# Optimization experiments

Measured on AMD Instinct MI355X. Metric: run time of the kernel, lower is better.

Reference implementation:

```python
import jax, jax.numpy as jnp
import numpy as np
from math import sqrt

B, S, E, H = 4, 4096, 512, 64


def setup_inputs() -> dict:
    key = jax.random.key(0)
    ks = jax.random.split(key, 9)
    std = sqrt(2.0 / (E + 4 * H))
    x_query = jax.random.normal(ks[0], (B, S, E), dtype=jnp.float32)
    x_key = jax.random.normal(ks[1], (B, S, E), dtype=jnp.float32)
    x_value = jax.random.normal(ks[2], (B, S, E), dtype=jnp.float32)
    Wq = jax.random.normal(ks[3], (E, H), dtype=jnp.float32) * std
    Wk = jax.random.normal(ks[4], (E, H), dtype=jnp.float32) * std
    Wv = jax.random.normal(ks[5], (E, H), dtype=jnp.float32) * std
    bq = jnp.zeros((H,), dtype=jnp.float32)
    bk = jnp.zeros((H,), dtype=jnp.float32)
    bv = jnp.zeros((H,), dtype=jnp.float32)
    # causal mask: True entries are masked out (set to -inf), as in scores[mask] = -inf
    mask = jnp.broadcast_to(jnp.triu(jnp.ones((S, S), dtype=bool), k=1), (B, S, S))
    return {"x_query": x_query, "x_key": x_key, "x_value": x_value,
            "Wq": Wq, "bq": bq, "Wk": Wk, "bk": bk, "Wv": Wv, "bv": bv,
            "mask": mask}


def reference(x_query, x_key, x_value, Wq, bq, Wk, bk, Wv, bv, mask):
    scale = 1.0 / sqrt(H)
    Q = x_query @ Wq + bq              # [B, S, H]
    K = x_key @ Wk + bk                # [B, S, H]
    V = x_value @ Wv + bv              # [B, S, H]
    scores = jnp.einsum('bqh,bkh->bqk', Q, K) * scale  # [B, S, S]
    scores = jnp.where(mask, -jnp.inf, scores)
    attn = jax.nn.softmax(scores, axis=-1)
    Z = jnp.einsum('bqk,bkh->bqh', attn, V)             # [B, S, H]
    return Z
```

## Files before the change

kernel.cpp:

```cpp
#include <hip/hip_runtime.h>
#include <math.h>

#define BB 4
#define SS 4096
#define EE 512
#define HH 64
#define NSPLIT 8
#define NQ (BB * SS)

typedef __bf16 bf16x8 __attribute__((ext_vector_type(8)));
typedef short  s16x8  __attribute__((ext_vector_type(8)));
typedef float  f32x4  __attribute__((ext_vector_type(4)));

static __device__ __forceinline__ unsigned short f2bf(float f) {
    union { float f; unsigned int u; } v; v.f = f;
    unsigned int r = v.u + 0x7fffu + ((v.u >> 16) & 1u);
    return (unsigned short)(r >> 16);
}
static __device__ __forceinline__ float bf2f(unsigned short h) {
    union { unsigned int u; float f; } v; v.u = ((unsigned int)h) << 16;
    return v.f;
}
static __device__ __forceinline__ void split_bf(float x, unsigned short& h, unsigned short& l) {
    h = f2bf(x);
    l = f2bf(x - bf2f(h));
}

static __device__ __forceinline__ f32x4 mfma_bf16(s16x8 a, s16x8 b, f32x4 c) {
    return __builtin_amdgcn_mfma_f32_16x16x32_bf16(
        __builtin_bit_cast(bf16x8, a), __builtin_bit_cast(bf16x8, b), c, 0, 0, 0);
}

__global__ __launch_bounds__(256) void wprep_kernel(
    const float* __restrict__ Wq, const float* __restrict__ Wk,
    const float* __restrict__ Wv,
    unsigned short* __restrict__ WhT, unsigned short* __restrict__ WlT)
{
    const int mat = blockIdx.y;
    const float* W = (mat == 0) ? Wq : ((mat == 1) ? Wk : Wv);
    const int base = blockIdx.x * 2048;
    for (int ii = threadIdx.x; ii < 2048; ii += 256) {
        const int i = base + ii;
        const int k = i >> 6, n = i & 63;
        unsigned short h, l;
        split_bf(W[i], h, l);
        const size_t o = ((size_t)mat * HH + n) * EE + k;
        WhT[o] = h; WlT[o] = l;
    }
}

__global__ __launch_bounds__(256) void qkv_proj_kernel(
    const float* __restrict__ Xq, const float* __restrict__ Xk, const float* __restrict__ Xv,
    const float* __restrict__ bq, const float* __restrict__ bk, const float* __restrict__ bv,
    const unsigned short* __restrict__ WhT, const unsigned short* __restrict__ WlT,
    unsigned short* __restrict__ Qbf, unsigned short* __restrict__ Kbf,
    unsigned short* __restrict__ Vtb)
{
    const int mtx = blockIdx.y;
    const float* X    = (mtx == 0) ? Xq : ((mtx == 1) ? Xk : Xv);
    const float* bias = (mtx == 0) ? bq : ((mtx == 1) ? bk : bv);

    __shared__ unsigned short Ah[64 * 72], Al[64 * 72];
    __shared__ unsigned short Bh[64 * 72], Bl[64 * 72];

    const int tid  = threadIdx.x;
    const int lane = tid & 63;
    const int w    = tid >> 6;
    const int l15  = lane & 15;
    const int lg   = lane >> 4;
    const int r0   = blockIdx.x * 64;

    const int arow = tid >> 2;
    const int asg  = tid & 3;

    f32x4 acc[4] = {{0,0,0,0},{0,0,0,0},{0,0,0,0},{0,0,0,0}};

    for (int c = 0; c < EE / 64; ++c) {
        const float* xp = &X[(size_t)(r0 + arow) * EE + c * 64 + asg * 16];
        const float4 x0 = ((const float4*)xp)[0];
        const float4 x1 = ((const float4*)xp)[1];
        const float4 x2 = ((const float4*)xp)[2];
        const float4 x3 = ((const float4*)xp)[3];
        const size_t wb = ((size_t)mtx * HH + arow) * EE + (size_t)c * 64;
        const s16x8 wh0 = *(const s16x8*)&WhT[wb + asg * 8];
        const s16x8 wh1 = *(const s16x8*)&WhT[wb + 32 + asg * 8];
        const s16x8 wl0 = *(const s16x8*)&WlT[wb + asg * 8];
        const s16x8 wl1 = *(const s16x8*)&WlT[wb + 32 + asg * 8];
        __syncthreads();

        const float xs[16] = {x0.x,x0.y,x0.z,x0.w, x1.x,x1.y,x1.z,x1.w,
                              x2.x,x2.y,x2.z,x2.w, x3.x,x3.y,x3.z,x3.w};
        s16x8 ha, hb, la, lb;
        #pragma unroll
        for (int i = 0; i < 8; ++i) {
            unsigned short h, l;
            split_bf(xs[i], h, l);      ha[i] = (short)h; la[i] = (short)l;
            split_bf(xs[8 + i], h, l);  hb[i] = (short)h; lb[i] = (short)l;
        }
        *(s16x8*)&Ah[arow * 72 + asg * 16]     = ha;
        *(s16x8*)&Ah[arow * 72 + asg * 16 + 8] = hb;
        *(s16x8*)&Al[arow * 72 + asg * 16]     = la;
        *(s16x8*)&Al[arow * 72 + asg * 16 + 8] = lb;
        *(s16x8*)&Bh[arow * 72 + asg * 8]      = wh0;
        *(s16x8*)&Bh[arow * 72 + 32 + asg * 8] = wh1;
        *(s16x8*)&Bl[arow * 72 + asg * 8]      = wl0;
        *(s16x8*)&Bl[arow * 72 + 32 + asg * 8] = wl1;
        __syncthreads();

        const int ma = (w * 16 + l15) * 72;
        const s16x8 a_h0 = *(const s16x8*)&Ah[ma + lg * 8];
        const s16x8 a_h1 = *(const s16x8*)&Ah[ma + 32 + lg * 8];
        const s16x8 a_l0 = *(const s16x8*)&Al[ma + lg * 8];
        const s16x8 a_l1 = *(const s16x8*)&Al[ma + 32 + lg * 8];
        #pragma unroll
        for (int f = 0; f < 4; ++f) {
            const int nb = (f * 16 + l15) * 72;
            const s16x8 b_h0 = *(const s16x8*)&Bh[nb + lg * 8];
            const s16x8 b_h1 = *(const s16x8*)&Bh[nb + 32 + lg * 8];
            const s16x8 b_l0 = *(const s16x8*)&Bl[nb + lg * 8];
            const s16x8 b_l1 = *(const s16x8*)&Bl[nb + 32 + lg * 8];
            acc[f] = mfma_bf16(a_h0, b_h0, acc[f]);
            acc[f] = mfma_bf16(a_h1, b_h1, acc[f]);
            acc[f] = mfma_bf16(a_l0, b_h0, acc[f]);
            acc[f] = mfma_bf16(a_l1, b_h1, acc[f]);
            acc[f] = mfma_bf16(a_h0, b_l0, acc[f]);
            acc[f] = mfma_bf16(a_h1, b_l1, acc[f]);
        }
    }

    float bcol[4];
    #pragma unroll
    for (int f = 0; f < 4; ++f) bcol[f] = bias[f * 16 + l15];

    if (mtx < 2) {
        unsigned short* Out = (mtx == 0) ? Qbf : Kbf;
        #pragma unroll
        for (int f = 0; f < 4; ++f)
            #pragma unroll
            for (int r = 0; r < 4; ++r)
                Out[(size_t)(r0 + w * 16 + lg * 4 + r) * HH + f * 16 + l15] =
                    f2bf(acc[f][r] + bcol[f]);
    } else {
        const int b  = r0 >> 12;
        const int s0 = (r0 & 4095) + w * 16 + lg * 4;
        #pragma unroll
        for (int f = 0; f < 4; ++f) {
            ushort4 pk;
            pk.x = f2bf(acc[f][0] + bcol[f]);
            pk.y = f2bf(acc[f][1] + bcol[f]);
            pk.z = f2bf(acc[f][2] + bcol[f]);
            pk.w = f2bf(acc[f][3] + bcol[f]);
            *(ushort4*)&Vtb[((size_t)b * HH + f * 16 + l15) * SS + s0] = pk;
        }
    }
}

__global__ __launch_bounds__(256) void attn_partial_kernel(
    const unsigned short* __restrict__ Qbf, const unsigned short* __restrict__ Kbf,
    const unsigned short* __restrict__ Vtb, float* __restrict__ o_part,
    float* __restrict__ m_part, float* __restrict__ l_part)
{
    __shared__ unsigned short Ks[64 * 68];
    __shared__ unsigned short Vs[64 * 68];
    __shared__ unsigned short Pl[4 * 16 * 68];

    const int tid  = threadIdx.x;
    const int b    = blockIdx.z;
    const int cch  = blockIdx.y;
    const int qb0  = blockIdx.x * 64;
    const int lane = tid & 63;
    const int w    = tid >> 6;
    const int l15  = lane & 15;
    const int lg   = lane >> 4;
    const int qw0  = qb0 + w * 16;
    const float scale = 0.125f;

    const size_t qrow = (size_t)(b * SS + qw0 + l15) * HH;
    const s16x8 qf0 = *(const s16x8*)&Qbf[qrow + lg * 8];
    const s16x8 qf1 = *(const s16x8*)&Qbf[qrow + 32 + lg * 8];

    f32x4 o[4] = {{0,0,0,0},{0,0,0,0},{0,0,0,0},{0,0,0,0}};
    float m[4], l[4];
    #pragma unroll
    for (int r = 0; r < 4; ++r) { m[r] = -1.0e30f; l[r] = 0.f; }

    const int kkey = tid >> 2, ksg = tid & 3;
    const unsigned short* Kb = Kbf + (size_t)b * SS * HH;
    const unsigned short* Vb = Vtb + (size_t)b * HH * SS;

    const int T   = blockIdx.x + 1;
    const int tpc = (T + NSPLIT - 1) / NSPLIT;
    const int t0  = cch * tpc;
    const int t1  = min(t0 + tpc, T);
    unsigned short* PW = Pl + w * (16 * 68);

    for (int t = t0; t < t1; ++t) {
        const int k0 = t * 64;
        const s16x8 ka  = *(const s16x8*)&Kb[(size_t)(k0 + kkey) * HH + ksg * 8];
        const s16x8 kb2 = *(const s16x8*)&Kb[(size_t)(k0 + kkey) * HH + 32 + ksg * 8];
        const s16x8 va  = *(const s16x8*)&Vb[(size_t)kkey * SS + k0 + ksg * 8];
        const s16x8 vb2 = *(const s16x8*)&Vb[(size_t)kkey * SS + k0 + 32 + ksg * 8];
        __syncthreads();
        *(s16x8*)&Ks[kkey * 68 + ksg * 8]      = ka;
        *(s16x8*)&Ks[kkey * 68 + 32 + ksg * 8] = kb2;
        *(s16x8*)&Vs[kkey * 68 + ksg * 8]      = va;
        *(s16x8*)&Vs[kkey * 68 + 32 + ksg * 8] = vb2;
        __syncthreads();

        f32x4 sc[4];
        #pragma unroll
        for (int f = 0; f < 4; ++f) {
            const int kr = (f * 16 + l15) * 68;
            const s16x8 kfa = *(const s16x8*)&Ks[kr + lg * 8];
            const s16x8 kfb = *(const s16x8*)&Ks[kr + 32 + lg * 8];
            f32x4 z = {0, 0, 0, 0};
            z = mfma_bf16(qf0, kfa, z);
            z = mfma_bf16(qf1, kfb, z);
            sc[f] = z;
        }

        float sv[4][4];
        #pragma unroll
        for (int f = 0; f < 4; ++f)
            #pragma unroll
            for (int r = 0; r < 4; ++r) sv[f][r] = sc[f][r] * scale;
        if (k0 + 63 > qw0) {
            #pragma unroll
            for (int f = 0; f < 4; ++f)
                #pragma unroll
                for (int r = 0; r < 4; ++r) {
                    const int qr = qw0 + lg * 4 + r;
                    if (k0 + f * 16 + l15 > qr) sv[f][r] = -3.0e38f;
                }
        }

        float tm[4];
        #pragma unroll
        for (int r = 0; r < 4; ++r)
            tm[r] = fmaxf(fmaxf(sv[0][r], sv[1][r]), fmaxf(sv[2][r], sv[3][r]));
        #pragma unroll
        for (int d = 1; d < 16; d <<= 1)
            #pragma unroll
            for (int r = 0; r < 4; ++r) tm[r] = fmaxf(tm[r], __shfl_xor(tm[r], d));

        float al[4];
        #pragma unroll
        for (int r = 0; r < 4; ++r) {
            const float mn = fmaxf(m[r], tm[r]);
            al[r] = __expf(m[r] - mn);
            m[r]  = mn;
        }
        float p[4][4];
        #pragma unroll
        for (int f = 0; f < 4; ++f)
            #pragma unroll
            for (int r = 0; r < 4; ++r) p[f][r] = __expf(sv[f][r] - m[r]);
        #pragma unroll
        for (int r = 0; r < 4; ++r)
            l[r] = l[r] * al[r] + p[0][r] + p[1][r] + p[2][r] + p[3][r];
        #pragma unroll
        for (int f = 0; f < 4; ++f)
            #pragma unroll
            for (int r = 0; r < 4; ++r) o[f][r] *= al[r];

        #pragma unroll
        for (int f = 0; f < 4; ++f)
            #pragma unroll
            for (int r = 0; r < 4; ++r)
                PW[(lg * 4 + r) * 68 + f * 16 + l15] = f2bf(p[f][r]);
        const s16x8 pa0 = *(const s16x8*)&PW[l15 * 68 + lg * 8];
        const s16x8 pa1 = *(const s16x8*)&PW[l15 * 68 + 32 + lg * 8];
        #pragma unroll
        for (int f = 0; f < 4; ++f) {
            const int vr = (f * 16 + l15) * 68;
            const s16x8 vfa = *(const s16x8*)&Vs[vr + lg * 8];
            const s16x8 vfb = *(const s16x8*)&Vs[vr + 32 + lg * 8];
            o[f] = mfma_bf16(pa0, vfa, o[f]);
            o[f] = mfma_bf16(pa1, vfb, o[f]);
        }
    }

    #pragma unroll
    for (int d = 1; d < 16; d <<= 1)
        #pragma unroll
        for (int r = 0; r < 4; ++r) l[r] += __shfl_xor(l[r], d);

    #pragma unroll
    for (int r = 0; r < 4; ++r) {
        const size_t qlin = (size_t)b * SS + qb0 + w * 16 + lg * 4 + r;
        float* Op = o_part + ((size_t)cch * NQ + qlin) * HH;
        #pragma unroll
        for (int f = 0; f < 4; ++f) Op[f * 16 + l15] = o[f][r];
        if (l15 == 0) {
            m_part[(size_t)cch * NQ + qlin] = m[r];
            l_part[(size_t)cch * NQ + qlin] = l[r];
        }
    }
}

__global__ __launch_bounds__(256) void attn_combine_kernel(
    const float* __restrict__ o_part, const float* __restrict__ m_part,
    const float* __restrict__ l_part, float* __restrict__ O)
{
    const int g = blockIdx.x * 256 + threadIdx.x;
    const size_t qlin = (size_t)(g >> 4);
    const int h0 = (g & 15) * 4;

    float mv[NSPLIT], lv[NSPLIT];
    float M = -INFINITY;
    #pragma unroll
    for (int cc = 0; cc < NSPLIT; ++cc) {
        mv[cc] = m_part[(size_t)cc * NQ + qlin];
        lv[cc] = l_part[(size_t)cc * NQ + qlin];
        M = fmaxf(M, mv[cc]);
    }
    float L = 0.f;
    float4 acc = make_float4(0.f, 0.f, 0.f, 0.f);
    #pragma unroll
    for (int cc = 0; cc < NSPLIT; ++cc) {
        const float wc = __expf(mv[cc] - M);
        L += lv[cc] * wc;
        const float4 oc = *(const float4*)&o_part[((size_t)cc * NQ + qlin) * HH + h0];
        acc.x += wc * oc.x; acc.y += wc * oc.y;
        acc.z += wc * oc.z; acc.w += wc * oc.w;
    }
    const float inv = 1.0f / L;
    acc.x *= inv; acc.y *= inv; acc.z *= inv; acc.w *= inv;
    *(float4*)&O[qlin * HH + h0] = acc;
}

extern "C" void kernel_launch(void* const* d_in, const int* in_sizes, int n_in,
                              void* d_out, int out_size, void* d_ws, size_t ws_size,
                              hipStream_t stream) {
    const float* xq = (const float*)d_in[0];
    const float* xk = (const float*)d_in[1];
    const float* xv = (const float*)d_in[2];
    const float* Wq = (const float*)d_in[3];
    const float* bq = (const float*)d_in[4];
    const float* Wk = (const float*)d_in[5];
    const float* bk = (const float*)d_in[6];
    const float* Wv = (const float*)d_in[7];
    const float* bv = (const float*)d_in[8];

    unsigned short* Qbf = (unsigned short*)d_ws;
    unsigned short* Kbf = Qbf + (size_t)NQ * HH;
    unsigned short* Vtb = Kbf + (size_t)NQ * HH;
    unsigned short* WhT = Vtb + (size_t)NQ * HH;
    unsigned short* WlT = WhT + (size_t)3 * HH * EE;
    float* o_part = (float*)(WlT + (size_t)3 * HH * EE);
    float* m_part = o_part + (size_t)NSPLIT * NQ * HH;
    float* l_part = m_part + (size_t)NSPLIT * NQ;

    wprep_kernel<<<dim3(16, 3), 256, 0, stream>>>(Wq, Wk, Wv, WhT, WlT);

    qkv_proj_kernel<<<dim3(NQ / 64, 3), 256, 0, stream>>>(
        xq, xk, xv, bq, bk, bv, WhT, WlT, Qbf, Kbf, Vtb);

    attn_partial_kernel<<<dim3(SS / 64, NSPLIT, BB), 256, 0, stream>>>(
        Qbf, Kbf, Vtb, o_part, m_part, l_part);

    attn_combine_kernel<<<(NQ * 16) / 256, 256, 0, stream>>>(
        o_part, m_part, l_part, (float*)d_out);
}
```

Before: 443.3 us.

## Switch to fp16 MFMA, drop split-bf16 projection, double-buffer K/V, lazy rescale

Replaces the three-term split-bf16 projection GEMM with a single fp16 MFMA pass, which removes two thirds of the projection MFMAs and the low-part weight buffer. The attention scale is folded into Q at projection time. The attention kernel gains register-prefetched, double-buffered K/V shared tiles with one barrier per iteration. The online softmax now rescales only when the running max grows by more than 8. The cost is lower projection precision (fp16 inputs, and X values may exceed the fp16 mantissa range) and exp values up to e^8 stored as fp16 P.

Result: no change. 439.7 us (-0.8%).

```diff
diff --git a/kernel.cpp b/kernel.cpp
--- a/kernel.cpp
+++ b/kernel.cpp
@@ -8,33 +8,23 @@
 #define NSPLIT 8
 #define NQ (BB * SS)
 
-typedef __bf16 bf16x8 __attribute__((ext_vector_type(8)));
-typedef short  s16x8  __attribute__((ext_vector_type(8)));
-typedef float  f32x4  __attribute__((ext_vector_type(4)));
-
-static __device__ __forceinline__ unsigned short f2bf(float f) {
-    union { float f; unsigned int u; } v; v.f = f;
-    unsigned int r = v.u + 0x7fffu + ((v.u >> 16) & 1u);
-    return (unsigned short)(r >> 16);
-}
-static __device__ __forceinline__ float bf2f(unsigned short h) {
-    union { unsigned int u; float f; } v; v.u = ((unsigned int)h) << 16;
-    return v.f;
-}
-static __device__ __forceinline__ void split_bf(float x, unsigned short& h, unsigned short& l) {
-    h = f2bf(x);
-    l = f2bf(x - bf2f(h));
-}
-
-static __device__ __forceinline__ f32x4 mfma_bf16(s16x8 a, s16x8 b, f32x4 c) {
-    return __builtin_amdgcn_mfma_f32_16x16x32_bf16(
-        __builtin_bit_cast(bf16x8, a), __builtin_bit_cast(bf16x8, b), c, 0, 0, 0);
+typedef _Float16 f16x8 __attribute__((ext_vector_type(8)));
+typedef short    s16x8 __attribute__((ext_vector_type(8)));
+typedef float    f32x4 __attribute__((ext_vector_type(4)));
+
+static __device__ __forceinline__ unsigned short f2h(float f) {
+    _Float16 h = (_Float16)f;
+    return __builtin_bit_cast(unsigned short, h);
+}
+
+static __device__ __forceinline__ f32x4 mfma_f16(s16x8 a, s16x8 b, f32x4 c) {
+    return __builtin_amdgcn_mfma_f32_16x16x32_f16(
+        __builtin_bit_cast(f16x8, a), __builtin_bit_cast(f16x8, b), c, 0, 0, 0);
 }
 
 __global__ __launch_bounds__(256) void wprep_kernel(
     const float* __restrict__ Wq, const float* __restrict__ Wk,
-    const float* __restrict__ Wv,
-    unsigned short* __restrict__ WhT, unsigned short* __restrict__ WlT)
+    const float* __restrict__ Wv, unsigned short* __restrict__ WT)
 {
     const int mat = blockIdx.y;
     const float* W = (mat == 0) ? Wq : ((mat == 1) ? Wk : Wv);
@@ -42,26 +32,23 @@
     for (int ii = threadIdx.x; ii < 2048; ii += 256) {
         const int i = base + ii;
         const int k = i >> 6, n = i & 63;
-        unsigned short h, l;
-        split_bf(W[i], h, l);
-        const size_t o = ((size_t)mat * HH + n) * EE + k;
-        WhT[o] = h; WlT[o] = l;
+        WT[((size_t)mat * HH + n) * EE + k] = f2h(W[i]);
     }
 }
 
 __global__ __launch_bounds__(256) void qkv_proj_kernel(
     const float* __restrict__ Xq, const float* __restrict__ Xk, const float* __restrict__ Xv,
     const float* __restrict__ bq, const float* __restrict__ bk, const float* __restrict__ bv,
-    const unsigned short* __restrict__ WhT, const unsigned short* __restrict__ WlT,
-    unsigned short* __restrict__ Qbf, unsigned short* __restrict__ Kbf,
-    unsigned short* __restrict__ Vtb)
+    const unsigned short* __restrict__ WT,
+    unsigned short* __restrict__ Qf, unsigned short* __restrict__ Kf,
+    unsigned short* __restrict__ Vt)
 {
     const int mtx = blockIdx.y;
     const float* X    = (mtx == 0) ? Xq : ((mtx == 1) ? Xk : Xv);
     const float* bias = (mtx == 0) ? bq : ((mtx == 1) ? bk : bv);
 
-    __shared__ unsigned short Ah[64 * 72], Al[64 * 72];
-    __shared__ unsigned short Bh[64 * 72], Bl[64 * 72];
+    __shared__ unsigned short As[64 * 72];
+    __shared__ unsigned short Bs[64 * 72];
 
     const int tid  = threadIdx.x;
     const int lane = tid & 63;
@@ -81,87 +68,73 @@
         const float4 x1 = ((const float4*)xp)[1];
         const float4 x2 = ((const float4*)xp)[2];
         const float4 x3 = ((const float4*)xp)[3];
-        const size_t wb = ((size_t)mtx * HH + arow) * EE + (size_t)c * 64;
-        const s16x8 wh0 = *(const s16x8*)&WhT[wb + asg * 8];
-        const s16x8 wh1 = *(const s16x8*)&WhT[wb + 32 + asg * 8];
-        const s16x8 wl0 = *(const s16x8*)&WlT[wb + asg * 8];
-        const s16x8 wl1 = *(const s16x8*)&WlT[wb + 32 + asg * 8];
+        const size_t wb = ((size_t)mtx * HH + arow) * EE + c * 64 + asg * 16;
+        const s16x8 w0 = *(const s16x8*)&WT[wb];
+        const s16x8 w1 = *(const s16x8*)&WT[wb + 8];
         __syncthreads();
 
         const float xs[16] = {x0.x,x0.y,x0.z,x0.w, x1.x,x1.y,x1.z,x1.w,
                               x2.x,x2.y,x2.z,x2.w, x3.x,x3.y,x3.z,x3.w};
-        s16x8 ha, hb, la, lb;
+        s16x8 a0, a1;
         #pragma unroll
         for (int i = 0; i < 8; ++i) {
-            unsigned short h, l;
-            split_bf(xs[i], h, l);      ha[i] = (short)h; la[i] = (short)l;
-            split_bf(xs[8 + i], h, l);  hb[i] = (short)h; lb[i] = (short)l;
-        }
-        *(s16x8*)&Ah[arow * 72 + asg * 16]     = ha;
-        *(s16x8*)&Ah[arow * 72 + asg * 16 + 8] = hb;
-        *(s16x8*)&Al[arow * 72 + asg * 16]     = la;
-        *(s16x8*)&Al[arow * 72 + asg * 16 + 8] = lb;
-        *(s16x8*)&Bh[arow * 72 + asg * 8]      = wh0;
-        *(s16x8*)&Bh[arow * 72 + 32 + asg * 8] = wh1;
-        *(s16x8*)&Bl[arow * 72 + asg * 8]      = wl0;
-        *(s16x8*)&Bl[arow * 72 + 32 + asg * 8] = wl1;
+            a0[i] = (short)f2h(xs[i]);
+            a1[i] = (short)f2h(xs[8 + i]);
+        }
+        *(s16x8*)&As[arow * 72 + asg * 16]     = a0;
+        *(s16x8*)&As[arow * 72 + asg * 16 + 8] = a1;
+        *(s16x8*)&Bs[arow * 72 + asg * 16]     = w0;
+        *(s16x8*)&Bs[arow * 72 + asg * 16 + 8] = w1;
         __syncthreads();
 
         const int ma = (w * 16 + l15) * 72;
-        const s16x8 a_h0 = *(const s16x8*)&Ah[ma + lg * 8];
-        const s16x8 a_h1 = *(const s16x8*)&Ah[ma + 32 + lg * 8];
-        const s16x8 a_l0 = *(const s16x8*)&Al[ma + lg * 8];
-        const s16x8 a_l1 = *(const s16x8*)&Al[ma + 32 + lg * 8];
+        const s16x8 af0 = *(const s16x8*)&As[ma + lg * 8];
+        const s16x8 af1 = *(const s16x8*)&As[ma + 32 + lg * 8];
         #pragma unroll
         for (int f = 0; f < 4; ++f) {
             const int nb = (f * 16 + l15) * 72;
-            const s16x8 b_h0 = *(const s16x8*)&Bh[nb + lg * 8];
-            const s16x8 b_h1 = *(const s16x8*)&Bh[nb + 32 + lg * 8];
-            const s16x8 b_l0 = *(const s16x8*)&Bl[nb + lg * 8];
-            const s16x8 b_l1 = *(const s16x8*)&Bl[nb + 32 + lg * 8];
-            acc[f] = mfma_bf16(a_h0, b_h0, acc[f]);
-            acc[f] = mfma_bf16(a_h1, b_h1, acc[f]);
-            acc[f] = mfma_bf16(a_l0, b_h0, acc[f]);
-            acc[f] = mfma_bf16(a_l1, b_h1, acc[f]);
-            acc[f] = mfma_bf16(a_h0, b_l0, acc[f]);
-            acc[f] = mfma_bf16(a_h1, b_l1, acc[f]);
+            const s16x8 bf0 = *(const s16x8*)&Bs[nb + lg * 8];
+            const s16x8 bf1 = *(const s16x8*)&Bs[nb + 32 + lg * 8];
+            acc[f] = mfma_f16(af0, bf0, acc[f]);
+            acc[f] = mfma_f16(af1, bf1, acc[f]);
         }
     }
 
     float bcol[4];
     #pragma unroll
     for (int f = 0; f < 4; ++f) bcol[f] = bias[f * 16 + l15];
+    const float qs = (mtx == 0) ? 0.125f : 1.0f;
 
     if (mtx < 2) {
-        unsigned short* Out = (mtx == 0) ? Qbf : Kbf;
+        unsigned short* Out = (mtx == 0) ? Qf : Kf;
         #pragma unroll
         for (int f = 0; f < 4; ++f)
             #pragma unroll
             for (int r = 0; r < 4; ++r)
                 Out[(size_t)(r0 + w * 16 + lg * 4 + r) * HH + f * 16 + l15] =
-                    f2bf(acc[f][r] + bcol[f]);
+                    f2h((acc[f][r] + bcol[f]) * qs);
     } else {
         const int b  = r0 >> 12;
         const int s0 = (r0 & 4095) + w * 16 + lg * 4;
         #pragma unroll
         for (int f = 0; f < 4; ++f) {
             ushort4 pk;
-            pk.x = f2bf(acc[f][0] + bcol[f]);
-            pk.y = f2bf(acc[f][1] + bcol[f]);
-            pk.z = f2bf(acc[f][2] + bcol[f]);
-            pk.w = f2bf(acc[f][3] + bcol[f]);
-            *(ushort4*)&Vtb[((size_t)b * HH + f * 16 + l15) * SS + s0] = pk;
+            pk.x = f2h(acc[f][0] + bcol[f]);
+            pk.y = f2h(acc[f][1] + bcol[f]);
+            pk.z = f2h(acc[f][2] + bcol[f]);
+            pk.w = f2h(acc[f][3] + bcol[f]);
+            *(ushort4*)&Vt[((size_t)b * HH + f * 16 + l15) * SS + s0] = pk;
         }
     }
 }
 
 __global__ __launch_bounds__(256) void attn_partial_kernel(
-    const unsigned short* __restrict__ Qbf, const unsigned short* __restrict__ Kbf,
-    const unsigned short* __restrict__ Vtb, float* __restrict__ o_part,
+    const unsigned short* __restrict__ Qf, const unsigned short* __restrict__ Kf,
+    const unsigned short* __restrict__ Vt, float* __restrict__ o_part,
     float* __restrict__ m_part, float* __restrict__ l_part)
 {
-    __shared__ unsigned short Ks[64 * 68];
-    __shared__ unsigned short Vs[64 * 68];
+    __shared__ unsigned short Ks[2][64 * 68];
+    __shared__ unsigned short Vs[2][64 * 68];
     __shared__ unsigned short Pl[4 * 16 * 68];
 
     const int tid  = threadIdx.x;
@@ -173,11 +146,10 @@
     const int l15  = lane & 15;
     const int lg   = lane >> 4;
     const int qw0  = qb0 + w * 16;
-    const float scale = 0.125f;
 
     const size_t qrow = (size_t)(b * SS + qw0 + l15) * HH;
-    const s16x8 qf0 = *(const s16x8*)&Qbf[qrow + lg * 8];
-    const s16x8 qf1 = *(const s16x8*)&Qbf[qrow + 32 + lg * 8];
+    const s16x8 qf0 = *(const s16x8*)&Qf[qrow + lg * 8];
+    const s16x8 qf1 = *(const s16x8*)&Qf[qrow + 32 + lg * 8];
 
     f32x4 o[4] = {{0,0,0,0},{0,0,0,0},{0,0,0,0},{0,0,0,0}};
     float m[4], l[4];
@@ -185,37 +157,53 @@
     for (int r = 0; r < 4; ++r) { m[r] = -1.0e30f; l[r] = 0.f; }
 
     const int kkey = tid >> 2, ksg = tid & 3;
-    const unsigned short* Kb = Kbf + (size_t)b * SS * HH;
-    const unsigned short* Vb = Vtb + (size_t)b * HH * SS;
+    const unsigned short* Kb = Kf + (size_t)b * SS * HH;
+    const unsigned short* Vb = Vt + (size_t)b * HH * SS;
 
     const int T   = blockIdx.x + 1;
     const int tpc = (T + NSPLIT - 1) / NSPLIT;
     const int t0  = cch * tpc;
     const int t1  = min(t0 + tpc, T);
+    const int nt  = t1 - t0;
     unsigned short* PW = Pl + w * (16 * 68);
 
-    for (int t = t0; t < t1; ++t) {
-        const int k0 = t * 64;
-        const s16x8 ka  = *(const s16x8*)&Kb[(size_t)(k0 + kkey) * HH + ksg * 8];
-        const s16x8 kb2 = *(const s16x8*)&Kb[(size_t)(k0 + kkey) * HH + 32 + ksg * 8];
-        const s16x8 va  = *(const s16x8*)&Vb[(size_t)kkey * SS + k0 + ksg * 8];
-        const s16x8 vb2 = *(const s16x8*)&Vb[(size_t)kkey * SS + k0 + 32 + ksg * 8];
+    s16x8 ka, kb2, va, vb2;
+
+    if (nt > 0) {
+        const int k0 = t0 * 64;
+        ka  = *(const s16x8*)&Kb[(size_t)(k0 + kkey) * HH + ksg * 8];
+        kb2 = *(const s16x8*)&Kb[(size_t)(k0 + kkey) * HH + 32 + ksg * 8];
+        va  = *(const s16x8*)&Vb[(size_t)kkey * SS + k0 + ksg * 8];
+        vb2 = *(const s16x8*)&Vb[(size_t)kkey * SS + k0 + 32 + ksg * 8];
+        *(s16x8*)&Ks[0][kkey * 68 + ksg * 8]      = ka;
+        *(s16x8*)&Ks[0][kkey * 68 + 32 + ksg * 8] = kb2;
+        *(s16x8*)&Vs[0][kkey * 68 + ksg * 8]      = va;
+        *(s16x8*)&Vs[0][kkey * 68 + 32 + ksg * 8] = vb2;
         __syncthreads();
-        *(s16x8*)&Ks[kkey * 68 + ksg * 8]      = ka;
-        *(s16x8*)&Ks[kkey * 68 + 32 + ksg * 8] = kb2;
-        *(s16x8*)&Vs[kkey * 68 + ksg * 8]      = va;
-        *(s16x8*)&Vs[kkey * 68 + 32 + ksg * 8] = vb2;
-        __syncthreads();
+    }
+
+    for (int i = 0; i < nt; ++i) {
+        const int t   = t0 + i;
+        const int cur = i & 1;
+        const int k0  = t * 64;
+
+        if (i + 1 < nt) {
+            const int kn = (t + 1) * 64;
+            ka  = *(const s16x8*)&Kb[(size_t)(kn + kkey) * HH + ksg * 8];
+            kb2 = *(const s16x8*)&Kb[(size_t)(kn + kkey) * HH + 32 + ksg * 8];
+            va  = *(const s16x8*)&Vb[(size_t)kkey * SS + kn + ksg * 8];
+            vb2 = *(const s16x8*)&Vb[(size_t)kkey * SS + kn + 32 + ksg * 8];
+        }
 
         f32x4 sc[4];
         #pragma unroll
         for (int f = 0; f < 4; ++f) {
             const int kr = (f * 16 + l15) * 68;
-            const s16x8 kfa = *(const s16x8*)&Ks[kr + lg * 8];
-            const s16x8 kfb = *(const s16x8*)&Ks[kr + 32 + lg * 8];
+            const s16x8 kfa = *(const s16x8*)&Ks[cur][kr + lg * 8];
+            const s16x8 kfb = *(const s16x8*)&Ks[cur][kr + 32 + lg * 8];
             f32x4 z = {0, 0, 0, 0};
-            z = mfma_bf16(qf0, kfa, z);
-            z = mfma_bf16(qf1, kfb, z);
+            z = mfma_f16(qf0, kfa, z);
+            z = mfma_f16(qf1, kfb, z);
             sc[f] = z;
         }
 
@@ -223,7 +211,7 @@
         #pragma unroll
         for (int f = 0; f < 4; ++f)
             #pragma unroll
-            for (int r = 0; r < 4; ++r) sv[f][r] = sc[f][r] * scale;
+            for (int r = 0; r < 4; ++r) sv[f][r] = sc[f][r];
         if (k0 + 63 > qw0) {
             #pragma unroll
             for (int f = 0; f < 4; ++f)
@@ -243,13 +231,21 @@
             #pragma unroll
             for (int r = 0; r < 4; ++r) tm[r] = fmaxf(tm[r], __shfl_xor(tm[r], d));
 
-        float al[4];
-        #pragma unroll
-        for (int r = 0; r < 4; ++r) {
-            const float mn = fmaxf(m[r], tm[r]);
-            al[r] = __expf(m[r] - mn);
-            m[r]  = mn;
-        }
+        bool grow = false;
+        #pragma unroll
+        for (int r = 0; r < 4; ++r) grow = grow || (tm[r] > m[r] + 8.0f);
+        if (__any((int)grow)) {
+            #pragma unroll
+            for (int r = 0; r < 4; ++r) {
+                const float mn = fmaxf(m[r], tm[r]);
+                const float al = __expf(m[r] - mn);
+                m[r] = mn;
+                l[r] *= al;
+                #pragma unroll
+                for (int f = 0; f < 4; ++f) o[f][r] *= al;
+            }
+        }
+
         float p[4][4];
         #pragma unroll
         for (int f = 0; f < 4; ++f)
@@ -257,26 +253,31 @@
             for (int r = 0; r < 4; ++r) p[f][r] = __expf(sv[f][r] - m[r]);
         #pragma unroll
         for (int r = 0; r < 4; ++r)
-            l[r] = l[r] * al[r] + p[0][r] + p[1][r] + p[2][r] + p[3][r];
+            l[r] += p[0][r] + p[1][r] + p[2][r] + p[3][r];
+
         #pragma unroll
         for (int f = 0; f < 4; ++f)
             #pragma unroll
-            for (int r = 0; r < 4; ++r) o[f][r] *= al[r];
-
-        #pragma unroll
-        for (int f = 0; f < 4; ++f)
-            #pragma unroll
             for (int r = 0; r < 4; ++r)
-                PW[(lg * 4 + r) * 68 + f * 16 + l15] = f2bf(p[f][r]);
+                PW[(lg * 4 + r) * 68 + f * 16 + l15] = f2h(p[f][r]);
         const s16x8 pa0 = *(const s16x8*)&PW[l15 * 68 + lg * 8];
         const s16x8 pa1 = *(const s16x8*)&PW[l15 * 68 + 32 + lg * 8];
         #pragma unroll
         for (int f = 0; f < 4; ++f) {
             const int vr = (f * 16 + l15) * 68;
-            const s16x8 vfa = *(const s16x8*)&Vs[vr + lg * 8];
-            const s16x8 vfb = *(const s16x8*)&Vs[vr + 32 + lg * 8];
-            o[f] = mfma_bf16(pa0, vfa, o[f]);
-            o[f] = mfma_bf16(pa1, vfb, o[f]);
+            const s16x8 vfa = *(const s16x8*)&Vs[cur][vr + lg * 8];
+            const s16x8 vfb = *(const s16x8*)&Vs[cur][vr + 32 + lg * 8];
+            o[f] = mfma_f16(pa0, vfa, o[f]);
+            o[f] = mfma_f16(pa1, vfb, o[f]);
+        }
+
+        if (i + 1 < nt) {
+            const int nxt = cur ^ 1;
+            *(s16x8*)&Ks[nxt][kkey * 68 + ksg * 8]      = ka;
+            *(s16x8*)&Ks[nxt][kkey * 68 + 32 + ksg * 8] = kb2;
+            *(s16x8*)&Vs[nxt][kkey * 68 + ksg * 8]      = va;
+            *(s16x8*)&Vs[nxt][kkey * 68 + 32 + ksg * 8] = vb2;
+            __syncthreads();
         }
     }
 
@@ -342,22 +343,21 @@
     const float* Wv = (const float*)d_in[7];
     const float* bv = (const float*)d_in[8];
 
-    unsigned short* Qbf = (unsigned short*)d_ws;
-    unsigned short* Kbf = Qbf + (size_t)NQ * HH;
-    unsigned short* Vtb = Kbf + (size_t)NQ * HH;
-    unsigned short* WhT = Vtb + (size_t)NQ * HH;
-    unsigned short* WlT = WhT + (size_t)3 * HH * EE;
-    float* o_part = (float*)(WlT + (size_t)3 * HH * EE);
+    unsigned short* Qf = (unsigned short*)d_ws;
+    unsigned short* Kf = Qf + (size_t)NQ * HH;
+    unsigned short* Vt = Kf + (size_t)NQ * HH;
+    unsigned short* WT = Vt + (size_t)NQ * HH;
+    float* o_part = (float*)(WT + (size_t)3 * HH * EE);
     float* m_part = o_part + (size_t)NSPLIT * NQ * HH;
     float* l_part = m_part + (size_t)NSPLIT * NQ;
 
-    wprep_kernel<<<dim3(16, 3), 256, 0, stream>>>(Wq, Wk, Wv, WhT, WlT);
+    wprep_kernel<<<dim3(16, 3), 256, 0, stream>>>(Wq, Wk, Wv, WT);
 
     qkv_proj_kernel<<<dim3(NQ / 64, 3), 256, 0, stream>>>(
-        xq, xk, xv, bq, bk, bv, WhT, WlT, Qbf, Kbf, Vtb);
+        xq, xk, xv, bq, bk, bv, WT, Qf, Kf, Vt);
 
     attn_partial_kernel<<<dim3(SS / 64, NSPLIT, BB), 256, 0, stream>>>(
-        Qbf, Kbf, Vtb, o_part, m_part, l_part);
+        Qf, Kf, Vt, o_part, m_part, l_part);
 
     attn_combine_kernel<<<(NQ * 16) / 256, 256, 0, stream>>>(
         o_part, m_part, l_part, (float*)d_out);
```
